# Kernel optimization log

Hardware: AMD Instinct MI355X
Metric: run time of the kernel (lower is better)

The kernel has to match this reference:

```python
import jax, jax.numpy as jnp
import numpy as np

B, T, D, H = 4, 2048, 768, 12
DH = D // H
SCALE = DH ** 0.5


def setup_inputs() -> dict:
    key = jax.random.key(0)
    k1, k2, k3, k4, k5, k6 = jax.random.split(key, 6)
    h = jax.random.normal(k1, (B, T, D), dtype=jnp.float32)
    key_padding_mask = jax.random.bernoulli(k2, 0.1, (B, T))
    s = 1.0 / np.sqrt(D)
    Wq = jax.random.normal(k3, (D, D), dtype=jnp.float32) * s
    Wk = jax.random.normal(k4, (D, D), dtype=jnp.float32) * s
    Wv = jax.random.normal(k5, (D, D), dtype=jnp.float32) * s
    Wo = jax.random.normal(k6, (D, D), dtype=jnp.float32) * s
    return {"h": h, "key_padding_mask": key_padding_mask,
            "Wq": Wq, "Wk": Wk, "Wv": Wv, "Wo": Wo}


def _split_heads(x):
    Bb, Tt, _ = x.shape
    return x.reshape(Bb, Tt, H, DH).transpose(0, 2, 1, 3)  # [B,H,T,Dh]


def reference(h, key_padding_mask, Wq, Wk, Wv, Wo):
    # torch nn.Linear (no bias): y = x @ W.T
    Q = _split_heads(h @ Wq.T)
    K = _split_heads(h @ Wk.T)
    V = _split_heads(h @ Wv.T)
    scores = jnp.einsum('bhqd,bhkd->bhqk', Q, K) / SCALE
    k_pad = key_padding_mask[:, None, None, :]  # mask padded keys
    q_pad = key_padding_mask[:, None, :, None]  # padded query rows
    scores = jnp.where(k_pad, jnp.float32(-1e9), scores)
    scores = jnp.where(q_pad, jnp.float32(0.0), scores)
    attn = jax.nn.softmax(scores, axis=-1)  # stable softmax (same math)
    attn = jnp.where(q_pad, jnp.float32(0.0), attn)
    out = jnp.einsum('bhqk,bhkd->bhqd', attn, V)  # [B,H,T,Dh]
    out = out.transpose(0, 2, 1, 3).reshape(B, T, D)
    return out @ Wo.T
```

## Files before the change

kernel.cpp:

```cpp
#include <hip/hip_runtime.h>
#include <stdint.h>

typedef __bf16 bf16x8 __attribute__((ext_vector_type(8)));
typedef float  f32x4  __attribute__((ext_vector_type(4)));
typedef unsigned short u16x4 __attribute__((ext_vector_type(4)));

#define MFMA16(a,b,c) __builtin_amdgcn_mfma_f32_16x16x32_bf16((a),(b),(c),0,0,0)

constexpr int Bc  = 4;
constexpr int Tc  = 2048;
constexpr int Dc  = 768;
constexpr int Hc  = 12;
constexpr int NTOK = Bc * Tc;
constexpr int QKV_LD = 3 * Dc;

static __device__ __forceinline__ unsigned short f2bf(float f){
  unsigned u = __float_as_uint(f);
  u += 0x7fffu + ((u >> 16) & 1u);
  return (unsigned short)(u >> 16);
}

static __device__ __forceinline__ float exp2a(float x){
  float r; asm("v_exp_f32 %0, %1" : "=v"(r) : "v"(x)); return r;
}

static __device__ __forceinline__ unsigned cvtpk_bf16(float lo, float hi){
  unsigned r; asm("v_cvt_pk_bf16_f32 %0, %1, %2" : "=v"(r) : "v"(lo), "v"(hi)); return r;
}

static __device__ __forceinline__ void gload_lds16(const void* g, void* l){
  __builtin_amdgcn_global_load_lds((__attribute__((address_space(1))) void*)g,
                                   (__attribute__((address_space(3))) void*)l,
                                   16, 0, 0);
}

__global__ void cvt_bf16(const float* __restrict__ src, unsigned short* __restrict__ dst,
                         int n4, float scale){
  int i = blockIdx.x * blockDim.x + threadIdx.x;
  if (i >= n4) return;
  float4 v = reinterpret_cast<const float4*>(src)[i];
  ushort4 o;
  o.x = f2bf(v.x * scale); o.y = f2bf(v.y * scale);
  o.z = f2bf(v.z * scale); o.w = f2bf(v.w * scale);
  reinterpret_cast<ushort4*>(dst)[i] = o;
}

__global__ void expand_mask(const unsigned* __restrict__ raw, int* __restrict__ out, int n){
  __shared__ int sInt, sFlt;
  int t = threadIdx.x;
  if (t == 0){ sInt = 1; sFlt = 1; }
  __syncthreads();
  int okI = 1, okF = 1;
  for (int i = t; i < n/4; i += blockDim.x){
    unsigned u = raw[i];
    okI &= (u <= 1u);
    okF &= (u == 0u || u == 0x3f800000u);
  }
  if (!okI) atomicAnd(&sInt, 0);
  if (!okF) atomicAnd(&sFlt, 0);
  __syncthreads();
  if (sInt || sFlt){
    for (int i = t; i < n; i += blockDim.x) out[i] = (raw[i] != 0u);
  } else {
    const unsigned char* rb = (const unsigned char*)raw;
    for (int i = t; i < n; i += blockDim.x) out[i] = (rb[i] != 0);
  }
}

template<typename CT>
__global__ __launch_bounds__(256) void gemm_bt(const unsigned short* __restrict__ A,
                                               const unsigned short* __restrict__ Bm,
                                               CT* __restrict__ C,
                                               int M, int N, int K){
  __shared__ unsigned short As[128*32];
  __shared__ unsigned short Bs[128*32];
  const int t = threadIdx.x;
  const int w = t >> 6, l = t & 63;
  const int wr = w >> 1, wc = w & 1;
  const int br = blockIdx.y * 128, bc = blockIdx.x * 128;

  f32x4 acc[4][4];
  const f32x4 fz = {0.f,0.f,0.f,0.f};
  #pragma unroll
  for (int m=0;m<4;m++)
    #pragma unroll
    for (int n=0;n<4;n++) acc[m][n] = fz;

  const int lrow = l >> 2;
  const int lk   = (l & 3) * 8;
  const int fr   = l & 15;
  const int fk   = (l >> 4) * 8;

  for (int k0 = 0; k0 < K; k0 += 32){
    #pragma unroll
    for (int it = 0; it < 2; ++it){
      const int rb = it*64 + w*16;
      gload_lds16(A  + (size_t)(br + rb + lrow)*K + k0 + lk, &As[rb*32]);
      gload_lds16(Bm + (size_t)(bc + rb + lrow)*K + k0 + lk, &Bs[rb*32]);
    }
    __syncthreads();
    bf16x8 a[4], b[4];
    #pragma unroll
    for (int m=0;m<4;m++)
      a[m] = *reinterpret_cast<const bf16x8*>(&As[(wr*64 + m*16 + fr)*32 + fk]);
    #pragma unroll
    for (int n=0;n<4;n++)
      b[n] = *reinterpret_cast<const bf16x8*>(&Bs[(wc*64 + n*16 + fr)*32 + fk]);
    #pragma unroll
    for (int m=0;m<4;m++)
      #pragma unroll
      for (int n=0;n<4;n++)
        acc[m][n] = MFMA16(a[m], b[n], acc[m][n]);
    __syncthreads();
  }

  const int orow0 = br + wr*64 + (l >> 4)*4;
  const int ocol0 = bc + wc*64 + (l & 15);
  #pragma unroll
  for (int m=0;m<4;m++)
    #pragma unroll
    for (int n=0;n<4;n++)
      #pragma unroll
      for (int r=0;r<4;r++){
        const size_t idx = (size_t)(orow0 + m*16 + r) * N + (ocol0 + n*16);
        float v = acc[m][n][r];
        if constexpr (sizeof(CT) == 2) C[idx] = (CT)f2bf(v);
        else                           C[idx] = v;
      }
}

__global__ __launch_bounds__(256, 4) void attn(const unsigned short* __restrict__ QKV,
                                               const int* __restrict__ mask,
                                               unsigned short* __restrict__ AO){
  __shared__ unsigned short Ks[64*64];
  __shared__ unsigned short Vt[64][72];
  __shared__ float Ms[64];

  const int t = threadIdx.x, w = t >> 6, l = t & 63;
  const int bh = blockIdx.y;
  const int b  = bh / Hc, h = bh - b * Hc;
  const int q0 = blockIdx.x * 128 + w * 32;
  const int fr = l & 15, fg = l >> 4;

  const size_t tokbase = (size_t)b * Tc;
  const unsigned short* Qp = QKV + (tokbase + q0) * (size_t)QKV_LD + h*64;
  const unsigned short* Kbase = QKV + tokbase * (size_t)QKV_LD + h*64 + 768;
  const unsigned short* Vbase = QKV + tokbase * (size_t)QKV_LD + h*64 + 1536;
  const int* bm = mask + b * Tc;

  bf16x8 qa[2][2];
  #pragma unroll
  for (int mc=0; mc<2; mc++)
    #pragma unroll
    for (int ks=0; ks<2; ks++)
      qa[mc][ks] = *reinterpret_cast<const bf16x8*>(
          Qp + (size_t)(mc*16+fr)*QKV_LD + ks*32 + fg*8);

  const f32x4 fz = {0.f,0.f,0.f,0.f};
  f32x4 accT[2][4];
  #pragma unroll
  for (int mc=0; mc<2; mc++)
    #pragma unroll
    for (int n=0; n<4; n++) accT[mc][n] = fz;
  float mrow[2] = {-1e30f, -1e30f};
  float lsum[2] = {0.f, 0.f};

  const int sg = t & 7;
  const int kp = t >> 3;

  union B8 { bf16x8 v; unsigned short s[8]; };

  for (int key0 = 0; key0 < Tc; key0 += 64){
    __syncthreads();
    #pragma unroll
    for (int i=0; i<2; i++)
      gload_lds16(Kbase + (size_t)(key0 + w*16 + i*8 + (l>>3))*QKV_LD + ((l&7)^(l>>3))*8,
                  &Ks[(w*16 + i*8)*64]);
    B8 v0, v1;
    v0.v = *reinterpret_cast<const bf16x8*>(Vbase + (size_t)(key0 + kp*2  )*QKV_LD + sg*8);
    v1.v = *reinterpret_cast<const bf16x8*>(Vbase + (size_t)(key0 + kp*2+1)*QKV_LD + sg*8);
    #pragma unroll
    for (int jr=0; jr<8; jr++){
      const int row = sg*8 + jr;
      ushort2 pr; pr.x = v0.s[jr]; pr.y = v1.s[jr];
      *reinterpret_cast<ushort2*>(&Vt[row][(kp*2) ^ (sg<<2)]) = pr;
    }
    if (t < 64) Ms[t] = bm[key0 + t] ? -1e9f : 0.f;
    __syncthreads();

    f32x4 S[2][4];
    #pragma unroll
    for (int g=0; g<4; g++){
      f32x4 mb = *reinterpret_cast<const f32x4*>(&Ms[g*16 + fg*4]);
      S[0][g] = mb; S[1][g] = mb;
      #pragma unroll
      for (int ks=0; ks<2; ks++){
        const int row = g*16 + fr;
        bf16x8 kf = *reinterpret_cast<const bf16x8*>(
            &Ks[row*64 + (((ks*4+fg) ^ (row&7))*8)]);
        S[0][g] = MFMA16(kf, qa[0][ks], S[0][g]);
        S[1][g] = MFMA16(kf, qa[1][ks], S[1][g]);
      }
    }

    unsigned pkAll[2][4][2];
    #pragma unroll
    for (int mc=0; mc<2; mc++){
      float cm = -3e38f;
      #pragma unroll
      for (int g=0; g<4; g++)
        cm = fmaxf(cm, fmaxf(fmaxf(S[mc][g][0], S[mc][g][1]),
                             fmaxf(S[mc][g][2], S[mc][g][3])));
      cm = fmaxf(cm, __shfl_xor(cm, 16));
      cm = fmaxf(cm, __shfl_xor(cm, 32));
      if (!__all(cm <= mrow[mc] + 8.0f)){
        const float nm = fmaxf(mrow[mc], cm);
        const float sc = exp2a(mrow[mc] - nm);
        lsum[mc] *= sc;
        #pragma unroll
        for (int n=0; n<4; n++) accT[mc][n] = accT[mc][n] * sc;
        mrow[mc] = nm;
      }
      float ps = 0.f;
      #pragma unroll
      for (int g=0; g<4; g++){
        const float p0 = exp2a(S[mc][g][0] - mrow[mc]);
        const float p1 = exp2a(S[mc][g][1] - mrow[mc]);
        const float p2 = exp2a(S[mc][g][2] - mrow[mc]);
        const float p3 = exp2a(S[mc][g][3] - mrow[mc]);
        ps += (p0 + p1) + (p2 + p3);
        pkAll[mc][g][0] = cvtpk_bf16(p0, p1);
        pkAll[mc][g][1] = cvtpk_bf16(p2, p3);
      }
      ps += __shfl_xor(ps, 16);
      ps += __shfl_xor(ps, 32);
      lsum[mc] += ps;
    }

    #pragma unroll
    for (int ks2=0; ks2<2; ks2++){
      union PBu { unsigned u[4]; bf16x8 v; } pb0, pb1;
      pb0.u[0] = pkAll[0][ks2*2][0];   pb0.u[1] = pkAll[0][ks2*2][1];
      pb0.u[2] = pkAll[0][ks2*2+1][0]; pb0.u[3] = pkAll[0][ks2*2+1][1];
      pb1.u[0] = pkAll[1][ks2*2][0];   pb1.u[1] = pkAll[1][ks2*2][1];
      pb1.u[2] = pkAll[1][ks2*2+1][0]; pb1.u[3] = pkAll[1][ks2*2+1][1];
      #pragma unroll
      for (int n=0; n<4; n++){
        const int row = n*16 + fr;
        const int sw  = (row>>3)<<2;
        union VA { u16x4 h[2]; bf16x8 v; } va;
        va.h[0] = *reinterpret_cast<const u16x4*>(&Vt[row][(ks2*32      + fg*4) ^ sw]);
        va.h[1] = *reinterpret_cast<const u16x4*>(&Vt[row][(ks2*32 + 16 + fg*4) ^ sw]);
        accT[0][n] = MFMA16(va.v, pb0.v, accT[0][n]);
        accT[1][n] = MFMA16(va.v, pb1.v, accT[1][n]);
      }
    }
  }

  #pragma unroll
  for (int mc=0; mc<2; mc++){
    const int qrow = q0 + mc*16 + fr;
    const int qm = bm[qrow];
    const float inv = (qm || lsum[mc] <= 0.f) ? 0.f : 1.f / lsum[mc];
    #pragma unroll
    for (int n=0; n<4; n++)
      #pragma unroll
      for (int r=0; r<4; r++)
        AO[(tokbase + qrow) * (size_t)Dc + h*64 + n*16 + fg*4 + r] =
            f2bf(accT[mc][n][r] * inv);
  }
}

extern "C" void kernel_launch(void* const* d_in, const int* in_sizes, int n_in,
                              void* d_out, int out_size, void* d_ws, size_t ws_size,
                              hipStream_t stream){
  const float* h    = (const float*)d_in[0];
  const unsigned* m = (const unsigned*)d_in[1];
  const float* Wq   = (const float*)d_in[2];
  const float* Wk   = (const float*)d_in[3];
  const float* Wv   = (const float*)d_in[4];
  const float* Wo   = (const float*)d_in[5];
  float* out        = (float*)d_out;

  unsigned short* hb   = (unsigned short*)d_ws;
  unsigned short* Wqkv = hb   + (size_t)NTOK * Dc;
  unsigned short* Wob  = Wqkv + (size_t)QKV_LD * Dc;
  unsigned short* QKV  = Wob  + (size_t)Dc * Dc;
  unsigned short* AO   = QKV  + (size_t)NTOK * QKV_LD;
  int* mexp            = (int*)(AO + (size_t)NTOK * Dc);

  const size_t need = ((size_t)NTOK*Dc + (size_t)QKV_LD*Dc + (size_t)Dc*Dc +
                       (size_t)NTOK*QKV_LD + (size_t)NTOK*Dc) * 2 + (size_t)NTOK*4;
  if (ws_size < need) return;

  const int W2 = Dc * Dc;
  cvt_bf16<<<(NTOK*Dc/4 + 255)/256, 256, 0, stream>>>(h,  hb,          NTOK*Dc/4, 1.0f);
  cvt_bf16<<<(W2/4 + 255)/256,      256, 0, stream>>>(Wq, Wqkv,        W2/4, 0.125f*1.44269504f);
  cvt_bf16<<<(W2/4 + 255)/256,      256, 0, stream>>>(Wk, Wqkv + W2,   W2/4, 1.0f);
  cvt_bf16<<<(W2/4 + 255)/256,      256, 0, stream>>>(Wv, Wqkv + 2*W2, W2/4, 1.0f);
  cvt_bf16<<<(W2/4 + 255)/256,      256, 0, stream>>>(Wo, Wob,         W2/4, 1.0f);
  expand_mask<<<1, 256, 0, stream>>>(m, mexp, NTOK);

  gemm_bt<unsigned short><<<dim3(QKV_LD/128, NTOK/128), 256, 0, stream>>>(
      hb, Wqkv, QKV, NTOK, QKV_LD, Dc);

  attn<<<dim3(Tc/128, Bc*Hc), 256, 0, stream>>>(QKV, mexp, AO);

  gemm_bt<float><<<dim3(Dc/128, NTOK/128), 256, 0, stream>>>(
      AO, Wob, out, NTOK, Dc, Dc);
}
```

Measured before the change: 187.7 us.

## Double-buffer K/V/mask tiles in attention loop with MFMA priority hints

Converts the attention kernel's single-buffered K, V-transpose and mask LDS tiles into double buffers. The next tile's global loads are issued after the QK^T MFMAs, and its V transpose is written to LDS after the PV MFMAs, so memory latency overlaps compute and one barrier per iteration is removed. It also raises wave priority around the MFMA sections. The cost is double the LDS use and a drop in launch-bounds occupancy from 4 to 3 blocks per CU.

```diff
diff --git a/kernel.cpp b/kernel.cpp
--- a/kernel.cpp
+++ b/kernel.cpp
@@ -129,12 +129,12 @@
       }
 }
 
-__global__ __launch_bounds__(256, 4) void attn(const unsigned short* __restrict__ QKV,
+__global__ __launch_bounds__(256, 3) void attn(const unsigned short* __restrict__ QKV,
                                                const int* __restrict__ mask,
                                                unsigned short* __restrict__ AO){
-  __shared__ unsigned short Ks[64*64];
-  __shared__ unsigned short Vt[64][72];
-  __shared__ float Ms[64];
+  __shared__ unsigned short Ks[2][64*64];
+  __shared__ unsigned short Vt[2][64][72];
+  __shared__ float Ms[2][64];
 
   const int t = threadIdx.x, w = t >> 6, l = t & 63;
   const int bh = blockIdx.y;
@@ -169,38 +169,54 @@
   const int kp = t >> 3;
 
   union B8 { bf16x8 v; unsigned short s[8]; };
-
-  for (int key0 = 0; key0 < Tc; key0 += 64){
+  B8 v0, v1;
+  int mv;
+
+  #pragma unroll
+  for (int i=0; i<2; i++)
+    gload_lds16(Kbase + (size_t)(w*16 + i*8 + (l>>3))*QKV_LD + ((l&7)^(l>>3))*8,
+                &Ks[0][(w*16 + i*8)*64]);
+  v0.v = *reinterpret_cast<const bf16x8*>(Vbase + (size_t)(kp*2  )*QKV_LD + sg*8);
+  v1.v = *reinterpret_cast<const bf16x8*>(Vbase + (size_t)(kp*2+1)*QKV_LD + sg*8);
+  mv = (t < 64) ? bm[t] : 0;
+  #pragma unroll
+  for (int jr=0; jr<8; jr++){
+    const int row = sg*8 + jr;
+    ushort2 pr; pr.x = v0.s[jr]; pr.y = v1.s[jr];
+    *reinterpret_cast<ushort2*>(&Vt[0][row][(kp*2) ^ (sg<<2)]) = pr;
+  }
+  if (t < 64) Ms[0][t] = mv ? -1e9f : 0.f;
+
+  for (int c = 0; c < Tc/64; ++c){
+    const int key0 = c * 64;
+    const int cur = c & 1;
     __syncthreads();
-    #pragma unroll
-    for (int i=0; i<2; i++)
-      gload_lds16(Kbase + (size_t)(key0 + w*16 + i*8 + (l>>3))*QKV_LD + ((l&7)^(l>>3))*8,
-                  &Ks[(w*16 + i*8)*64]);
-    B8 v0, v1;
-    v0.v = *reinterpret_cast<const bf16x8*>(Vbase + (size_t)(key0 + kp*2  )*QKV_LD + sg*8);
-    v1.v = *reinterpret_cast<const bf16x8*>(Vbase + (size_t)(key0 + kp*2+1)*QKV_LD + sg*8);
-    #pragma unroll
-    for (int jr=0; jr<8; jr++){
-      const int row = sg*8 + jr;
-      ushort2 pr; pr.x = v0.s[jr]; pr.y = v1.s[jr];
-      *reinterpret_cast<ushort2*>(&Vt[row][(kp*2) ^ (sg<<2)]) = pr;
-    }
-    if (t < 64) Ms[t] = bm[key0 + t] ? -1e9f : 0.f;
-    __syncthreads();
 
     f32x4 S[2][4];
+    __builtin_amdgcn_s_setprio(1);
     #pragma unroll
     for (int g=0; g<4; g++){
-      f32x4 mb = *reinterpret_cast<const f32x4*>(&Ms[g*16 + fg*4]);
+      f32x4 mb = *reinterpret_cast<const f32x4*>(&Ms[cur][g*16 + fg*4]);
       S[0][g] = mb; S[1][g] = mb;
       #pragma unroll
       for (int ks=0; ks<2; ks++){
         const int row = g*16 + fr;
         bf16x8 kf = *reinterpret_cast<const bf16x8*>(
-            &Ks[row*64 + (((ks*4+fg) ^ (row&7))*8)]);
+            &Ks[cur][row*64 + (((ks*4+fg) ^ (row&7))*8)]);
         S[0][g] = MFMA16(kf, qa[0][ks], S[0][g]);
         S[1][g] = MFMA16(kf, qa[1][ks], S[1][g]);
       }
+    }
+    __builtin_amdgcn_s_setprio(0);
+
+    if (c < Tc/64 - 1){
+      #pragma unroll
+      for (int i=0; i<2; i++)
+        gload_lds16(Kbase + (size_t)(key0+64 + w*16 + i*8 + (l>>3))*QKV_LD + ((l&7)^(l>>3))*8,
+                    &Ks[cur^1][(w*16 + i*8)*64]);
+      v0.v = *reinterpret_cast<const bf16x8*>(Vbase + (size_t)(key0+64 + kp*2  )*QKV_LD + sg*8);
+      v1.v = *reinterpret_cast<const bf16x8*>(Vbase + (size_t)(key0+64 + kp*2+1)*QKV_LD + sg*8);
+      mv = (t < 64) ? bm[key0+64 + t] : 0;
     }
 
     unsigned pkAll[2][4][2];
@@ -237,6 +253,7 @@
       lsum[mc] += ps;
     }
 
+    __builtin_amdgcn_s_setprio(1);
     #pragma unroll
     for (int ks2=0; ks2<2; ks2++){
       union PBu { unsigned u[4]; bf16x8 v; } pb0, pb1;
@@ -249,11 +266,22 @@
         const int row = n*16 + fr;
         const int sw  = (row>>3)<<2;
         union VA { u16x4 h[2]; bf16x8 v; } va;
-        va.h[0] = *reinterpret_cast<const u16x4*>(&Vt[row][(ks2*32      + fg*4) ^ sw]);
-        va.h[1] = *reinterpret_cast<const u16x4*>(&Vt[row][(ks2*32 + 16 + fg*4) ^ sw]);
+        va.h[0] = *reinterpret_cast<const u16x4*>(&Vt[cur][row][(ks2*32      + fg*4) ^ sw]);
+        va.h[1] = *reinterpret_cast<const u16x4*>(&Vt[cur][row][(ks2*32 + 16 + fg*4) ^ sw]);
         accT[0][n] = MFMA16(va.v, pb0.v, accT[0][n]);
         accT[1][n] = MFMA16(va.v, pb1.v, accT[1][n]);
       }
+    }
+    __builtin_amdgcn_s_setprio(0);
+
+    if (c < Tc/64 - 1){
+      #pragma unroll
+      for (int jr=0; jr<8; jr++){
+        const int row = sg*8 + jr;
+        ushort2 pr; pr.x = v0.s[jr]; pr.y = v1.s[jr];
+        *reinterpret_cast<ushort2*>(&Vt[cur^1][row][(kp*2) ^ (sg<<2)]) = pr;
+      }
+      if (t < 64) Ms[cur^1][t] = mv ? -1e9f : 0.f;
     }
   }
 
```

Result: faster. 183.7 us (-2.1%).

## Pre-transpose V globally and triple-buffer K/V tiles with async LDS loads

Applied to the files above, without the earlier changes.

Adds a separate kernel that transposes V into a per-head [d][token] buffer (reusing the hb workspace), so the attention kernel can bring V into shared memory with direct global-to-LDS loads instead of register shuffles. The attention loop becomes a three-stage ring of K/V/mask buffers, prefetched two chunks ahead and synchronised with explicit waitcnt plus barrier. It also precomputes the key mask as bits, raises MFMA priority with setprio, and vectorises the output stores. In exchange it pays for an extra kernel launch and a V round trip through memory, and uses more LDS, which lowers the occupancy bound from 4 to 3.

```diff
diff --git a/kernel.cpp b/kernel.cpp
--- a/kernel.cpp
+++ b/kernel.cpp
@@ -129,12 +129,43 @@
       }
 }
 
-__global__ __launch_bounds__(256, 4) void attn(const unsigned short* __restrict__ QKV,
+__global__ __launch_bounds__(256) void vtrans(const unsigned short* __restrict__ QKV,
+                                              unsigned short* __restrict__ VtG){
+  __shared__ unsigned short st[64][72];
+  const int t = threadIdx.x;
+  const int token0 = blockIdx.x * 64;
+  const int bh = blockIdx.y;
+  const int b = bh / Hc, h = bh - b * Hc;
+  const size_t tokbase = (size_t)b * Tc;
+
+  const int tok = t >> 2;
+  const unsigned short* src = QKV + (tokbase + token0 + tok) * (size_t)QKV_LD + 1536 + h*64;
+  #pragma unroll
+  for (int i = 0; i < 2; ++i){
+    const int ul = (t & 3)*2 + i;
+    *reinterpret_cast<uint4*>(&st[tok][ul*8]) =
+        *reinterpret_cast<const uint4*>(src + ul*8);
+  }
+  __syncthreads();
+  const int d = t >> 2;
+  #pragma unroll
+  for (int half = 0; half < 2; ++half){
+    union { unsigned short s[8]; uint4 q; } tmp;
+    const int tk0 = (t & 3)*8 + half*32;
+    #pragma unroll
+    for (int j = 0; j < 8; ++j)
+      tmp.s[j] = st[tk0 + j][d];
+    *reinterpret_cast<uint4*>(VtG + ((size_t)(bh*64 + d))*Tc + token0 + tk0) = tmp.q;
+  }
+}
+
+__global__ __launch_bounds__(256, 3) void attn(const unsigned short* __restrict__ QKV,
+                                               const unsigned short* __restrict__ VtG,
                                                const int* __restrict__ mask,
                                                unsigned short* __restrict__ AO){
-  __shared__ unsigned short Ks[64*64];
-  __shared__ unsigned short Vt[64][72];
-  __shared__ float Ms[64];
+  __shared__ unsigned short Ks[3][64*64];
+  __shared__ unsigned short Vs[3][64*64];
+  __shared__ float Ms[3][64];
 
   const int t = threadIdx.x, w = t >> 6, l = t & 63;
   const int bh = blockIdx.y;
@@ -145,7 +176,7 @@
   const size_t tokbase = (size_t)b * Tc;
   const unsigned short* Qp = QKV + (tokbase + q0) * (size_t)QKV_LD + h*64;
   const unsigned short* Kbase = QKV + tokbase * (size_t)QKV_LD + h*64 + 768;
-  const unsigned short* Vbase = QKV + tokbase * (size_t)QKV_LD + h*64 + 1536;
+  const unsigned short* VtB = VtG + (size_t)(bh*64) * Tc;
   const int* bm = mask + b * Tc;
 
   bf16x8 qa[2][2];
@@ -156,6 +187,13 @@
       qa[mc][ks] = *reinterpret_cast<const bf16x8*>(
           Qp + (size_t)(mc*16+fr)*QKV_LD + ks*32 + fg*8);
 
+  unsigned bits = 0;
+  if (w == 0){
+    #pragma unroll
+    for (int cc = 0; cc < 32; ++cc)
+      bits |= (unsigned)(bm[cc*64 + l] != 0) << cc;
+  }
+
   const f32x4 fz = {0.f,0.f,0.f,0.f};
   f32x4 accT[2][4];
   #pragma unroll
@@ -165,43 +203,53 @@
   float mrow[2] = {-1e30f, -1e30f};
   float lsum[2] = {0.f, 0.f};
 
-  const int sg = t & 7;
-  const int kp = t >> 3;
-
-  union B8 { bf16x8 v; unsigned short s[8]; };
-
-  for (int key0 = 0; key0 < Tc; key0 += 64){
-    __syncthreads();
-    #pragma unroll
-    for (int i=0; i<2; i++)
-      gload_lds16(Kbase + (size_t)(key0 + w*16 + i*8 + (l>>3))*QKV_LD + ((l&7)^(l>>3))*8,
-                  &Ks[(w*16 + i*8)*64]);
-    B8 v0, v1;
-    v0.v = *reinterpret_cast<const bf16x8*>(Vbase + (size_t)(key0 + kp*2  )*QKV_LD + sg*8);
-    v1.v = *reinterpret_cast<const bf16x8*>(Vbase + (size_t)(key0 + kp*2+1)*QKV_LD + sg*8);
-    #pragma unroll
-    for (int jr=0; jr<8; jr++){
-      const int row = sg*8 + jr;
-      ushort2 pr; pr.x = v0.s[jr]; pr.y = v1.s[jr];
-      *reinterpret_cast<ushort2*>(&Vt[row][(kp*2) ^ (sg<<2)]) = pr;
-    }
-    if (t < 64) Ms[t] = bm[key0 + t] ? -1e9f : 0.f;
-    __syncthreads();
+  const int srow = l >> 3, scol = (l & 7) ^ (l >> 3);
+  auto stage = [&](int c){
+    const int key0 = c * 64, buf = c % 3;
+    #pragma unroll
+    for (int i=0; i<2; i++){
+      const int rb = w*16 + i*8;
+      gload_lds16(Kbase + (size_t)(key0 + rb + srow)*QKV_LD + scol*8,
+                  &Ks[buf][rb*64]);
+    }
+    #pragma unroll
+    for (int i=0; i<2; i++){
+      const int rb = (w*2 + i)*8;
+      gload_lds16(VtB + (size_t)(rb + srow)*Tc + key0 + scol*8,
+                  &Vs[buf][rb*64]);
+    }
+  };
+
+  stage(0); stage(1);
+  if (w == 0){
+    Ms[0][l] = (bits & 1u) ? -1e9f : 0.f;
+    Ms[1][l] = (bits & 2u) ? -1e9f : 0.f;
+  }
+  asm volatile("s_waitcnt vmcnt(4) lgkmcnt(0)" ::: "memory");
+  __builtin_amdgcn_s_barrier();
+  asm volatile("" ::: "memory");
+
+  for (int c = 0; c < 32; ++c){
+    const int cb = c % 3;
 
     f32x4 S[2][4];
+    __builtin_amdgcn_s_setprio(1);
     #pragma unroll
     for (int g=0; g<4; g++){
-      f32x4 mb = *reinterpret_cast<const f32x4*>(&Ms[g*16 + fg*4]);
+      f32x4 mb = *reinterpret_cast<const f32x4*>(&Ms[cb][g*16 + fg*4]);
       S[0][g] = mb; S[1][g] = mb;
       #pragma unroll
       for (int ks=0; ks<2; ks++){
         const int row = g*16 + fr;
         bf16x8 kf = *reinterpret_cast<const bf16x8*>(
-            &Ks[row*64 + (((ks*4+fg) ^ (row&7))*8)]);
+            &Ks[cb][row*64 + (((ks*4+fg) ^ (row&7))*8)]);
         S[0][g] = MFMA16(kf, qa[0][ks], S[0][g]);
         S[1][g] = MFMA16(kf, qa[1][ks], S[1][g]);
       }
     }
+    __builtin_amdgcn_s_setprio(0);
+
+    if (c + 2 < 32) stage(c + 2);
 
     unsigned pkAll[2][4][2];
     #pragma unroll
@@ -237,6 +285,7 @@
       lsum[mc] += ps;
     }
 
+    __builtin_amdgcn_s_setprio(1);
     #pragma unroll
     for (int ks2=0; ks2<2; ks2++){
       union PBu { unsigned u[4]; bf16x8 v; } pb0, pb1;
@@ -247,13 +296,25 @@
       #pragma unroll
       for (int n=0; n<4; n++){
         const int row = n*16 + fr;
-        const int sw  = (row>>3)<<2;
         union VA { u16x4 h[2]; bf16x8 v; } va;
-        va.h[0] = *reinterpret_cast<const u16x4*>(&Vt[row][(ks2*32      + fg*4) ^ sw]);
-        va.h[1] = *reinterpret_cast<const u16x4*>(&Vt[row][(ks2*32 + 16 + fg*4) ^ sw]);
+        va.h[0] = *reinterpret_cast<const u16x4*>(
+            &Vs[cb][row*64 + (((ks2*4     + (fg>>1)) ^ (row&7))*8) + (fg&1)*4]);
+        va.h[1] = *reinterpret_cast<const u16x4*>(
+            &Vs[cb][row*64 + (((ks2*4 + 2 + (fg>>1)) ^ (row&7))*8) + (fg&1)*4]);
         accT[0][n] = MFMA16(va.v, pb0.v, accT[0][n]);
         accT[1][n] = MFMA16(va.v, pb1.v, accT[1][n]);
       }
+    }
+    __builtin_amdgcn_s_setprio(0);
+
+    if (w == 0 && c + 2 < 32)
+      Ms[(c+2)%3][l] = ((bits >> (c+2)) & 1u) ? -1e9f : 0.f;
+
+    if (c < 31){
+      if (c < 30) asm volatile("s_waitcnt vmcnt(4) lgkmcnt(0)" ::: "memory");
+      else        asm volatile("s_waitcnt vmcnt(0) lgkmcnt(0)" ::: "memory");
+      __builtin_amdgcn_s_barrier();
+      asm volatile("" ::: "memory");
     }
   }
 
@@ -263,11 +324,15 @@
     const int qm = bm[qrow];
     const float inv = (qm || lsum[mc] <= 0.f) ? 0.f : 1.f / lsum[mc];
     #pragma unroll
-    for (int n=0; n<4; n++)
-      #pragma unroll
-      for (int r=0; r<4; r++)
-        AO[(tokbase + qrow) * (size_t)Dc + h*64 + n*16 + fg*4 + r] =
-            f2bf(accT[mc][n][r] * inv);
+    for (int n=0; n<4; n++){
+      ushort4 o;
+      o.x = f2bf(accT[mc][n][0] * inv);
+      o.y = f2bf(accT[mc][n][1] * inv);
+      o.z = f2bf(accT[mc][n][2] * inv);
+      o.w = f2bf(accT[mc][n][3] * inv);
+      *reinterpret_cast<ushort4*>(
+          &AO[(tokbase + qrow) * (size_t)Dc + h*64 + n*16 + fg*4]) = o;
+    }
   }
 }
 
@@ -304,7 +369,10 @@
   gemm_bt<unsigned short><<<dim3(QKV_LD/128, NTOK/128), 256, 0, stream>>>(
       hb, Wqkv, QKV, NTOK, QKV_LD, Dc);
 
-  attn<<<dim3(Tc/128, Bc*Hc), 256, 0, stream>>>(QKV, mexp, AO);
+  unsigned short* VtG = hb;
+  vtrans<<<dim3(Tc/64, Bc*Hc), 256, 0, stream>>>(QKV, VtG);
+
+  attn<<<dim3(Tc/128, Bc*Hc), 256, 0, stream>>>(QKV, VtG, mexp, AO);
 
   gemm_bt<float><<<dim3(Dc/128, NTOK/128), 256, 0, stream>>>(
       AO, Wob, out, NTOK, Dc, Dc);
```

Result: slower. 192.3 us (+2.5%).
